# Performance work log

Measured on AMD Instinct MI355X. Metric: run time of the kernel, lower is better.

The kernel has to match this reference:

```python
import jax, jax.numpy as jnp
import numpy as np

TEMPERATURE = 0.07


def setup_inputs() -> dict:
    key = jax.random.key(0)
    k1, k2 = jax.random.split(key)
    features = jax.random.normal(k1, (8192, 512), dtype=jnp.float32)
    targets = jax.random.randint(k2, (8192,), 0, 100, dtype=jnp.int64)
    return {"features": features, "targets": targets}


def reference(features, targets):
    n = features.shape[0]
    # L2 normalize along feature dim (F.normalize, dim=1)
    feats = features / jnp.linalg.norm(features, axis=1, keepdims=True)
    # [N, N] similarity matrix
    sim = jnp.matmul(feats, feats.T) / TEMPERATURE
    # positive-pair mask (same label, excluding self)
    mask = (targets[:, None] == targets[None, :]).astype(sim.dtype)
    mask = mask - jnp.eye(n, dtype=sim.dtype)
    # log_prob = sim - log(sum_j exp(sim_ij)) ; denominator includes the diagonal,
    # exactly as in the torch code. logsumexp is the stable single-pass form.
    log_prob = sim - jax.nn.logsumexp(sim, axis=1, keepdims=True)
    mean_log_prob_pos = jnp.sum(mask * log_prob, axis=1) / jnp.sum(mask, axis=1)
    loss = -jnp.mean(mean_log_prob_pos)
    return loss
```

## Files before the change

kernel.cpp:

```cpp
#include <hip/hip_runtime.h>

#define BM 128
#define BN 128
#define HBN 64
#define NSPLIT 8
#define TEMP 0.07f

typedef __attribute__((ext_vector_type(4))) float f32x4;
typedef __attribute__((ext_vector_type(4))) int   i32x4;
typedef __attribute__((ext_vector_type(8))) int   i32x8;

__global__ __launch_bounds__(256) void knorm(const float* __restrict__ X,
                                             unsigned char* __restrict__ Fq, int D) {
  int row = blockIdx.x * 4 + (threadIdx.x >> 6);
  int lane = threadIdx.x & 63;
  const float4* xr = (const float4*)(X + (size_t)row * D);
  float4 a = xr[lane * 2];
  float4 b = xr[lane * 2 + 1];
  float ss = a.x*a.x + a.y*a.y + a.z*a.z + a.w*a.w
           + b.x*b.x + b.y*b.y + b.z*b.z + b.w*b.w;
  #pragma unroll
  for (int off = 1; off < 64; off <<= 1) ss += __shfl_xor(ss, off, 64);
  float r = rsqrtf(ss);
  int lo = 0, hi = 0;
  lo = __builtin_amdgcn_cvt_pk_fp8_f32(a.x*r, a.y*r, lo, false);
  lo = __builtin_amdgcn_cvt_pk_fp8_f32(a.z*r, a.w*r, lo, true);
  hi = __builtin_amdgcn_cvt_pk_fp8_f32(b.x*r, b.y*r, hi, false);
  hi = __builtin_amdgcn_cvt_pk_fp8_f32(b.z*r, b.w*r, hi, true);
  int2 o = make_int2(lo, hi);
  *(int2*)(Fq + (size_t)row * D + lane * 8) = o;
}

__global__ __launch_bounds__(256, 1)
void kmain(const unsigned char* __restrict__ F, const int* __restrict__ tgt,
           float* __restrict__ psum, float* __restrict__ pmask, int N, int D) {
  __shared__ __align__(16) unsigned char Bs[2][HBN * 512];
  __shared__ int tgts[1024];

  const int tid  = threadIdx.x;
  const int lane = tid & 63;
  const int wave = tid >> 6;
  const int quad = lane >> 4;
  const int l15  = lane & 15;

  const int rowblk   = blockIdx.x / NSPLIT;
  const int split    = blockIdx.x % NSPLIT;
  const int rowbase  = rowblk * BM;
  const int colbase0 = split * (N / NSPLIT);
  const int NS       = N / NSPLIT;
  const int GT       = NS / HBN;

  i32x8 af[2][4];
  #pragma unroll
  for (int mi = 0; mi < 2; ++mi) {
    const unsigned char* rp = F + (size_t)(rowbase + wave*32 + mi*16 + l15) * 512 + quad*32;
    #pragma unroll
    for (int ks = 0; ks < 4; ++ks) {
      i32x4 lo = *(const i32x4*)(rp + ks*128);
      i32x4 hi = *(const i32x4*)(rp + ks*128 + 16);
      af[mi][ks] = __builtin_shufflevector(lo, hi, 0,1,2,3,4,5,6,7);
    }
  }

  int trow[2][4];
  #pragma unroll
  for (int mi = 0; mi < 2; ++mi)
    #pragma unroll
    for (int r = 0; r < 4; ++r)
      trow[mi][r] = tgt[rowbase + wave*32 + mi*16 + quad*4 + r];

  for (int i = tid; i < NS; i += 256) tgts[i] = tgt[colbase0 + i];

  float se[2][4], ms[2][4];
  #pragma unroll
  for (int mi = 0; mi < 2; ++mi)
    #pragma unroll
    for (int r = 0; r < 4; ++r) { se[mi][r] = 0.f; ms[mi][r] = 0.f; }

  const float C1 = (1.0f / TEMP) * 1.4426950408889634f;
  const float C0 = -C1;

  auto STAGE = [&](int g, int buf) {
    const int cb = colbase0 + g * HBN;
    #pragma unroll
    for (int it = 0; it < 8; ++it) {
      const int L   = it * 256 + tid;
      const int row = L >> 5;
      const int ks  = (L & 31) ^ (row & 7);
      const unsigned char* gp = F + (size_t)(cb + row) * 512 + ks * 16;
      __builtin_amdgcn_global_load_lds(
          (const __attribute__((address_space(1))) void*)gp,
          (__attribute__((address_space(3))) void*)(&Bs[buf][0] + L * 16), 16, 0, 0);
    }
  };

  const int sw0 = (quad * 2) ^ (l15 & 7);

  __syncthreads();

  STAGE(0, 0);

  for (int g = 0; g < GT; ++g) {
    if (g + 1 < GT) {
      STAGE(g + 1, (g + 1) & 1);
      asm volatile("s_waitcnt vmcnt(8)" ::: "memory");
    } else {
      asm volatile("s_waitcnt vmcnt(0)" ::: "memory");
    }
    __builtin_amdgcn_s_barrier();

    f32x4 acc[2][4];
    #pragma unroll
    for (int mi = 0; mi < 2; ++mi)
      #pragma unroll
      for (int ni = 0; ni < 4; ++ni)
        acc[mi][ni] = (f32x4){0.f, 0.f, 0.f, 0.f};

    const unsigned char* bb  = &Bs[0][0] + (g & 1) * (HBN * 512) + l15 * 512;
    const unsigned char* bp0 = bb + sw0 * 16;
    const unsigned char* bp1 = bb + (sw0 ^ 1) * 16;

    #pragma unroll
    for (int ks = 0; ks < 4; ++ks) {
      #pragma unroll
      for (int ni = 0; ni < 4; ++ni) {
        i32x4 b0 = *(const i32x4*)(bp0 + ni*8192 + ks*128);
        i32x4 b1 = *(const i32x4*)(bp1 + ni*8192 + ks*128);
        i32x8 b = __builtin_shufflevector(b0, b1, 0,1,2,3,4,5,6,7);
        acc[0][ni] = __builtin_amdgcn_mfma_scale_f32_16x16x128_f8f6f4(
            af[0][ks], b, acc[0][ni], 0, 0, 0, 0x7F7F7F7F, 0, 0x7F7F7F7F);
        acc[1][ni] = __builtin_amdgcn_mfma_scale_f32_16x16x128_f8f6f4(
            af[1][ks], b, acc[1][ni], 0, 0, 0, 0x7F7F7F7F, 0, 0x7F7F7F7F);
      }
    }
    __builtin_amdgcn_s_barrier();

    int tc[4];
    #pragma unroll
    for (int ni = 0; ni < 4; ++ni) tc[ni] = tgts[g*HBN + ni*16 + l15];
    #pragma unroll
    for (int mi = 0; mi < 2; ++mi)
      #pragma unroll
      for (int ni = 0; ni < 4; ++ni)
        #pragma unroll
        for (int r = 0; r < 4; ++r) {
          float v = acc[mi][ni][r];
          se[mi][r] += __builtin_amdgcn_exp2f(fmaf(v, C1, C0));
          if (tc[ni] == trow[mi][r]) ms[mi][r] += v;
        }
  }

  #pragma unroll
  for (int mi = 0; mi < 2; ++mi)
    #pragma unroll
    for (int r = 0; r < 4; ++r) {
      float s = se[mi][r], m = ms[mi][r];
      #pragma unroll
      for (int off = 1; off < 16; off <<= 1) {
        s += __shfl_xor(s, off, 64);
        m += __shfl_xor(m, off, 64);
      }
      if (l15 == 0) {
        int row = rowbase + wave*32 + mi*16 + quad*4 + r;
        psum[(size_t)split * N + row]  = s;
        pmask[(size_t)split * N + row] = m;
      }
    }
}

__global__ __launch_bounds__(256) void kfinal(
    const float* __restrict__ psum, const float* __restrict__ pmask,
    const int* __restrict__ tgt, float* __restrict__ out, int N) {
  __shared__ int h[128];
  __shared__ float wsum[4];
  const int tid = threadIdx.x;
  if (tid < 128) h[tid] = 0;
  __syncthreads();
  for (int i = tid; i < N; i += 256) atomicAdd(&h[tgt[i] & 127], 1);
  __syncthreads();

  const int i = blockIdx.x * 256 + tid;
  float s = 0.f, m = 0.f;
  #pragma unroll
  for (int sp = 0; sp < NSPLIT; ++sp) {
    s += psum[(size_t)sp * N + i];
    m += pmask[(size_t)sp * N + i];
  }
  const float invT = 1.0f / TEMP;
  float cnt = (float)(h[tgt[i] & 127] - 1);
  float term = (m - 1.0f) * invT / cnt - (logf(s) + invT);
  #pragma unroll
  for (int off = 1; off < 64; off <<= 1) term += __shfl_xor(term, off, 64);
  if ((tid & 63) == 0) wsum[tid >> 6] = term;
  __syncthreads();
  if (tid == 0)
    atomicAdd(out, -(wsum[0] + wsum[1] + wsum[2] + wsum[3]) / (float)N);
}

extern "C" void kernel_launch(void* const* d_in, const int* in_sizes, int n_in,
                              void* d_out, int out_size, void* d_ws, size_t ws_size,
                              hipStream_t stream) {
  const float* X  = (const float*)d_in[0];
  const int* tgt  = (const int*)d_in[1];
  float* out      = (float*)d_out;
  const int N = in_sizes[1];
  const int D = in_sizes[0] / N;

  char* w = (char*)d_ws;
  unsigned char* Fq = (unsigned char*)w;
  size_t off = (size_t)N * D;
  float* psum  = (float*)(w + off); off += (size_t)NSPLIT * N * sizeof(float);
  float* pmask = (float*)(w + off);

  hipMemsetAsync(d_out, 0, sizeof(float), stream);
  knorm<<<N / 4, 256, 0, stream>>>(X, Fq, D);
  kmain<<<(N / BM) * NSPLIT, 256, 0, stream>>>(Fq, tgt, psum, pmask, N, D);
  kfinal<<<N / 256, 256, 0, stream>>>(psum, pmask, tgt, out, N);
}
```

Baseline: 114.9 us.

## Exploit similarity symmetry: compute only upper-triangular tiles with column-side reductions

The main kernel now computes only the upper-triangular 128x128 tile pairs of the symmetric similarity matrix. Each tile produces row sums for block I and, when off-diagonal, column sums for block J, written into per-block partial slots, which roughly halves the MFMA and exp work. In exchange there are more, smaller blocks, each loading a 128-column tile up front without a pipelined loop, plus extra column reductions through LDS. The final kernel now sums over 64 partial slots instead of 8, and the normalization kernel uses a coalesced row layout.

After: 151.4 us. 1.32x slower.

```diff
diff --git a/kernel.cpp b/kernel.cpp
--- a/kernel.cpp
+++ b/kernel.cpp
@@ -1,9 +1,7 @@
 #include <hip/hip_runtime.h>
 
 #define BM 128
-#define BN 128
 #define HBN 64
-#define NSPLIT 8
 #define TEMP 0.07f
 
 typedef __attribute__((ext_vector_type(4))) float f32x4;
@@ -15,8 +13,8 @@
   int row = blockIdx.x * 4 + (threadIdx.x >> 6);
   int lane = threadIdx.x & 63;
   const float4* xr = (const float4*)(X + (size_t)row * D);
-  float4 a = xr[lane * 2];
-  float4 b = xr[lane * 2 + 1];
+  float4 a = xr[lane];
+  float4 b = xr[lane + 64];
   float ss = a.x*a.x + a.y*a.y + a.z*a.z + a.w*a.w
            + b.x*b.x + b.y*b.y + b.z*b.z + b.w*b.w;
   #pragma unroll
@@ -27,15 +25,16 @@
   lo = __builtin_amdgcn_cvt_pk_fp8_f32(a.z*r, a.w*r, lo, true);
   hi = __builtin_amdgcn_cvt_pk_fp8_f32(b.x*r, b.y*r, hi, false);
   hi = __builtin_amdgcn_cvt_pk_fp8_f32(b.z*r, b.w*r, hi, true);
-  int2 o = make_int2(lo, hi);
-  *(int2*)(Fq + (size_t)row * D + lane * 8) = o;
+  unsigned char* op = Fq + (size_t)row * D;
+  *(int*)(op + lane * 4)       = lo;
+  *(int*)(op + 256 + lane * 4) = hi;
 }
 
 __global__ __launch_bounds__(256, 1)
 void kmain(const unsigned char* __restrict__ F, const int* __restrict__ tgt,
            float* __restrict__ psum, float* __restrict__ pmask, int N, int D) {
   __shared__ __align__(16) unsigned char Bs[2][HBN * 512];
-  __shared__ int tgts[1024];
+  __shared__ float cred[2][4][128];
 
   const int tid  = threadIdx.x;
   const int lane = tid & 63;
@@ -43,12 +42,21 @@
   const int quad = lane >> 4;
   const int l15  = lane & 15;
 
-  const int rowblk   = blockIdx.x / NSPLIT;
-  const int split    = blockIdx.x % NSPLIT;
-  const int rowbase  = rowblk * BM;
-  const int colbase0 = split * (N / NSPLIT);
-  const int NS       = N / NSPLIT;
-  const int GT       = NS / HBN;
+  const int NBLK = N / BM;
+  const int half = NBLK >> 1;
+  const int base = NBLK * half;
+  int I, J;
+  if ((int)blockIdx.x < base) {
+    int t = blockIdx.x / NBLK;
+    I = blockIdx.x - t * NBLK;
+    J = I + t; if (J >= NBLK) J -= NBLK;
+  } else {
+    I = blockIdx.x - base;
+    J = I + half;
+  }
+  const bool diag = (I == J);
+  const int rowbase = I * BM;
+  const int colbase = J * BM;
 
   i32x8 af[2][4];
   #pragma unroll
@@ -69,46 +77,37 @@
     for (int r = 0; r < 4; ++r)
       trow[mi][r] = tgt[rowbase + wave*32 + mi*16 + quad*4 + r];
 
-  for (int i = tid; i < NS; i += 256) tgts[i] = tgt[colbase0 + i];
+  int tc0[4], tc1[4];
+  #pragma unroll
+  for (int ni = 0; ni < 4; ++ni) {
+    tc0[ni] = tgt[colbase + ni*16 + l15];
+    tc1[ni] = tgt[colbase + 64 + ni*16 + l15];
+  }
+
+  #pragma unroll
+  for (int it = 0; it < 16; ++it) {
+    const int L   = it * 256 + tid;
+    const int row = L >> 5;
+    const int ks  = (L & 31) ^ (row & 7);
+    const unsigned char* gp = F + (size_t)(colbase + row) * 512 + ks * 16;
+    __builtin_amdgcn_global_load_lds(
+        (const __attribute__((address_space(1))) void*)gp,
+        (__attribute__((address_space(3))) void*)(&Bs[0][0] + L * 16), 16, 0, 0);
+  }
 
   float se[2][4], ms[2][4];
   #pragma unroll
   for (int mi = 0; mi < 2; ++mi)
     #pragma unroll
     for (int r = 0; r < 4; ++r) { se[mi][r] = 0.f; ms[mi][r] = 0.f; }
+  f32x4 ce0 = (f32x4){0,0,0,0}, ce1 = (f32x4){0,0,0,0};
+  f32x4 cm0 = (f32x4){0,0,0,0}, cm1 = (f32x4){0,0,0,0};
 
   const float C1 = (1.0f / TEMP) * 1.4426950408889634f;
   const float C0 = -C1;
-
-  auto STAGE = [&](int g, int buf) {
-    const int cb = colbase0 + g * HBN;
-    #pragma unroll
-    for (int it = 0; it < 8; ++it) {
-      const int L   = it * 256 + tid;
-      const int row = L >> 5;
-      const int ks  = (L & 31) ^ (row & 7);
-      const unsigned char* gp = F + (size_t)(cb + row) * 512 + ks * 16;
-      __builtin_amdgcn_global_load_lds(
-          (const __attribute__((address_space(1))) void*)gp,
-          (__attribute__((address_space(3))) void*)(&Bs[buf][0] + L * 16), 16, 0, 0);
-    }
-  };
-
   const int sw0 = (quad * 2) ^ (l15 & 7);
 
-  __syncthreads();
-
-  STAGE(0, 0);
-
-  for (int g = 0; g < GT; ++g) {
-    if (g + 1 < GT) {
-      STAGE(g + 1, (g + 1) & 1);
-      asm volatile("s_waitcnt vmcnt(8)" ::: "memory");
-    } else {
-      asm volatile("s_waitcnt vmcnt(0)" ::: "memory");
-    }
-    __builtin_amdgcn_s_barrier();
-
+  auto PHASE = [&](const int g, f32x4& ceg, f32x4& cmg, const int (&tcg)[4]) {
     f32x4 acc[2][4];
     #pragma unroll
     for (int mi = 0; mi < 2; ++mi)
@@ -116,7 +115,7 @@
       for (int ni = 0; ni < 4; ++ni)
         acc[mi][ni] = (f32x4){0.f, 0.f, 0.f, 0.f};
 
-    const unsigned char* bb  = &Bs[0][0] + (g & 1) * (HBN * 512) + l15 * 512;
+    const unsigned char* bb  = &Bs[0][0] + g * (HBN * 512) + l15 * 512;
     const unsigned char* bp0 = bb + sw0 * 16;
     const unsigned char* bp1 = bb + (sw0 ^ 1) * 16;
 
@@ -133,11 +132,7 @@
             af[1][ks], b, acc[1][ni], 0, 0, 0, 0x7F7F7F7F, 0, 0x7F7F7F7F);
       }
     }
-    __builtin_amdgcn_s_barrier();
-
-    int tc[4];
-    #pragma unroll
-    for (int ni = 0; ni < 4; ++ni) tc[ni] = tgts[g*HBN + ni*16 + l15];
+
     #pragma unroll
     for (int mi = 0; mi < 2; ++mi)
       #pragma unroll
@@ -145,10 +140,19 @@
         #pragma unroll
         for (int r = 0; r < 4; ++r) {
           float v = acc[mi][ni][r];
-          se[mi][r] += __builtin_amdgcn_exp2f(fmaf(v, C1, C0));
-          if (tc[ni] == trow[mi][r]) ms[mi][r] += v;
+          float e = __builtin_amdgcn_exp2f(fmaf(v, C1, C0));
+          se[mi][r] += e;
+          ceg[ni]   += e;
+          if (tcg[ni] == trow[mi][r]) { ms[mi][r] += v; cmg[ni] += v; }
         }
-  }
+  };
+
+  asm volatile("s_waitcnt vmcnt(8)" ::: "memory");
+  __builtin_amdgcn_s_barrier();
+  PHASE(0, ce0, cm0, tc0);
+  asm volatile("s_waitcnt vmcnt(0)" ::: "memory");
+  __builtin_amdgcn_s_barrier();
+  PHASE(1, ce1, cm1, tc1);
 
   #pragma unroll
   for (int mi = 0; mi < 2; ++mi)
@@ -162,15 +166,38 @@
       }
       if (l15 == 0) {
         int row = rowbase + wave*32 + mi*16 + quad*4 + r;
-        psum[(size_t)split * N + row]  = s;
-        pmask[(size_t)split * N + row] = m;
+        psum [(size_t)J * N + row] = s;
+        pmask[(size_t)J * N + row] = m;
       }
     }
+
+  if (!diag) {
+    #pragma unroll
+    for (int g = 0; g < 2; ++g)
+      #pragma unroll
+      for (int ni = 0; ni < 4; ++ni) {
+        float e = g ? ce1[ni] : ce0[ni];
+        float m = g ? cm1[ni] : cm0[ni];
+        e += __shfl_xor(e, 16, 64); e += __shfl_xor(e, 32, 64);
+        m += __shfl_xor(m, 16, 64); m += __shfl_xor(m, 32, 64);
+        if (quad == 0) {
+          cred[0][wave][g*64 + ni*16 + l15] = e;
+          cred[1][wave][g*64 + ni*16 + l15] = m;
+        }
+      }
+  }
+  __syncthreads();
+  if (!diag && tid < 128) {
+    float s = cred[0][0][tid] + cred[0][1][tid] + cred[0][2][tid] + cred[0][3][tid];
+    float m = cred[1][0][tid] + cred[1][1][tid] + cred[1][2][tid] + cred[1][3][tid];
+    psum [(size_t)I * N + colbase + tid] = s;
+    pmask[(size_t)I * N + colbase + tid] = m;
+  }
 }
 
 __global__ __launch_bounds__(256) void kfinal(
     const float* __restrict__ psum, const float* __restrict__ pmask,
-    const int* __restrict__ tgt, float* __restrict__ out, int N) {
+    const int* __restrict__ tgt, float* __restrict__ out, int N, int nslot) {
   __shared__ int h[128];
   __shared__ float wsum[4];
   const int tid = threadIdx.x;
@@ -181,8 +208,8 @@
 
   const int i = blockIdx.x * 256 + tid;
   float s = 0.f, m = 0.f;
-  #pragma unroll
-  for (int sp = 0; sp < NSPLIT; ++sp) {
+  #pragma unroll 8
+  for (int sp = 0; sp < nslot; ++sp) {
     s += psum[(size_t)sp * N + i];
     m += pmask[(size_t)sp * N + i];
   }
@@ -205,15 +232,17 @@
   float* out      = (float*)d_out;
   const int N = in_sizes[1];
   const int D = in_sizes[0] / N;
+  const int NBLK = N / BM;
+  const int grid2 = NBLK * (NBLK + 1) / 2;
 
   char* w = (char*)d_ws;
   unsigned char* Fq = (unsigned char*)w;
   size_t off = (size_t)N * D;
-  float* psum  = (float*)(w + off); off += (size_t)NSPLIT * N * sizeof(float);
+  float* psum  = (float*)(w + off); off += (size_t)NBLK * N * sizeof(float);
   float* pmask = (float*)(w + off);
 
   hipMemsetAsync(d_out, 0, sizeof(float), stream);
   knorm<<<N / 4, 256, 0, stream>>>(X, Fq, D);
-  kmain<<<(N / BM) * NSPLIT, 256, 0, stream>>>(Fq, tgt, psum, pmask, N, D);
-  kfinal<<<N / 256, 256, 0, stream>>>(psum, pmask, tgt, out, N);
-}
+  kmain<<<grid2, 256, 0, stream>>>(Fq, tgt, psum, pmask, N, D);
+  kfinal<<<N / 256, 256, 0, stream>>>(psum, pmask, tgt, out, N, NBLK);
+}
```

## Software-pipeline exp epilogue behind next tile's MFMAs, fold memset into norm kernel

Applied to the files above, without the earlier changes.

The main loop now processes the previous tile's accumulators (exp2 and the positive-mask sum) at the top of the next iteration, so the transcendental work can overlap with the MFMA issue of the current tile. The MFMA block is raised to high wave priority with s_setprio. A dummy zero tile in the first iteration is cancelled by subtracting its exp contribution at the end. The norm kernel also zeroes the output, which removes the separate memset launch, and it uses coalesced float4 loads with a permuted fp8 column order. That permutation is the same for every row, so the dot products are unchanged. The cost is more live registers for the carried accumulators, and the dummy-subtraction trick adds a small floating-point error.

Result: no change. 116.1 us (+1.0%).

```diff
diff --git a/kernel.cpp b/kernel.cpp
--- a/kernel.cpp
+++ b/kernel.cpp
@@ -1,7 +1,6 @@
 #include <hip/hip_runtime.h>
 
 #define BM 128
-#define BN 128
 #define HBN 64
 #define NSPLIT 8
 #define TEMP 0.07f
@@ -11,12 +10,14 @@
 typedef __attribute__((ext_vector_type(8))) int   i32x8;
 
 __global__ __launch_bounds__(256) void knorm(const float* __restrict__ X,
-                                             unsigned char* __restrict__ Fq, int D) {
+                                             unsigned char* __restrict__ Fq,
+                                             float* __restrict__ out, int D) {
+  if (blockIdx.x == 0 && threadIdx.x == 0) *out = 0.f;
   int row = blockIdx.x * 4 + (threadIdx.x >> 6);
   int lane = threadIdx.x & 63;
   const float4* xr = (const float4*)(X + (size_t)row * D);
-  float4 a = xr[lane * 2];
-  float4 b = xr[lane * 2 + 1];
+  float4 a = xr[lane];
+  float4 b = xr[lane + 64];
   float ss = a.x*a.x + a.y*a.y + a.z*a.z + a.w*a.w
            + b.x*b.x + b.y*b.y + b.z*b.z + b.w*b.w;
   #pragma unroll
@@ -27,8 +28,9 @@
   lo = __builtin_amdgcn_cvt_pk_fp8_f32(a.z*r, a.w*r, lo, true);
   hi = __builtin_amdgcn_cvt_pk_fp8_f32(b.x*r, b.y*r, hi, false);
   hi = __builtin_amdgcn_cvt_pk_fp8_f32(b.z*r, b.w*r, hi, true);
-  int2 o = make_int2(lo, hi);
-  *(int2*)(Fq + (size_t)row * D + lane * 8) = o;
+  unsigned char* op = Fq + (size_t)row * D;
+  *(int*)(op + lane * 4)       = lo;
+  *(int*)(op + 256 + lane * 4) = hi;
 }
 
 __global__ __launch_bounds__(256, 1)
@@ -96,6 +98,16 @@
 
   const int sw0 = (quad * 2) ^ (l15 & 7);
 
+  f32x4 accP[2][4];
+  int   tcP[4];
+  #pragma unroll
+  for (int mi = 0; mi < 2; ++mi)
+    #pragma unroll
+    for (int ni = 0; ni < 4; ++ni)
+      accP[mi][ni] = (f32x4){0.f, 0.f, 0.f, 0.f};
+  #pragma unroll
+  for (int ni = 0; ni < 4; ++ni) tcP[ni] = trow[0][0];
+
   __syncthreads();
 
   STAGE(0, 0);
@@ -109,6 +121,17 @@
     }
     __builtin_amdgcn_s_barrier();
 
+    #pragma unroll
+    for (int mi = 0; mi < 2; ++mi)
+      #pragma unroll
+      for (int ni = 0; ni < 4; ++ni)
+        #pragma unroll
+        for (int r = 0; r < 4; ++r) {
+          float v = accP[mi][ni][r];
+          se[mi][r] += __builtin_amdgcn_exp2f(fmaf(v, C1, C0));
+          if (tcP[ni] == trow[mi][r]) ms[mi][r] += v;
+        }
+
     f32x4 acc[2][4];
     #pragma unroll
     for (int mi = 0; mi < 2; ++mi)
@@ -120,6 +143,7 @@
     const unsigned char* bp0 = bb + sw0 * 16;
     const unsigned char* bp1 = bb + (sw0 ^ 1) * 16;
 
+    __builtin_amdgcn_s_setprio(1);
     #pragma unroll
     for (int ks = 0; ks < 4; ++ks) {
       #pragma unroll
@@ -133,21 +157,35 @@
             af[1][ks], b, acc[1][ni], 0, 0, 0, 0x7F7F7F7F, 0, 0x7F7F7F7F);
       }
     }
+    __builtin_amdgcn_s_setprio(0);
+
+    #pragma unroll
+    for (int mi = 0; mi < 2; ++mi)
+      #pragma unroll
+      for (int ni = 0; ni < 4; ++ni)
+        accP[mi][ni] = acc[mi][ni];
+    #pragma unroll
+    for (int ni = 0; ni < 4; ++ni) tcP[ni] = tgts[g*HBN + ni*16 + l15];
+
     __builtin_amdgcn_s_barrier();
-
-    int tc[4];
-    #pragma unroll
-    for (int ni = 0; ni < 4; ++ni) tc[ni] = tgts[g*HBN + ni*16 + l15];
-    #pragma unroll
-    for (int mi = 0; mi < 2; ++mi)
-      #pragma unroll
-      for (int ni = 0; ni < 4; ++ni)
-        #pragma unroll
-        for (int r = 0; r < 4; ++r) {
-          float v = acc[mi][ni][r];
-          se[mi][r] += __builtin_amdgcn_exp2f(fmaf(v, C1, C0));
-          if (tc[ni] == trow[mi][r]) ms[mi][r] += v;
-        }
+  }
+
+  #pragma unroll
+  for (int mi = 0; mi < 2; ++mi)
+    #pragma unroll
+    for (int ni = 0; ni < 4; ++ni)
+      #pragma unroll
+      for (int r = 0; r < 4; ++r) {
+        float v = accP[mi][ni][r];
+        se[mi][r] += __builtin_amdgcn_exp2f(fmaf(v, C1, C0));
+        if (tcP[ni] == trow[mi][r]) ms[mi][r] += v;
+      }
+  {
+    float dummy = 16.0f * __builtin_amdgcn_exp2f(C0);
+    #pragma unroll
+    for (int mi = 0; mi < 2; ++mi)
+      #pragma unroll
+      for (int r = 0; r < 4; ++r) se[mi][r] -= dummy;
   }
 
   #pragma unroll
@@ -212,8 +250,7 @@
   float* psum  = (float*)(w + off); off += (size_t)NSPLIT * N * sizeof(float);
   float* pmask = (float*)(w + off);
 
-  hipMemsetAsync(d_out, 0, sizeof(float), stream);
-  knorm<<<N / 4, 256, 0, stream>>>(X, Fq, D);
+  knorm<<<N / 4, 256, 0, stream>>>(X, Fq, out, D);
   kmain<<<(N / BM) * NSPLIT, 256, 0, stream>>>(Fq, tgt, psum, pmask, N, D);
   kfinal<<<N / 256, 256, 0, stream>>>(psum, pmask, tgt, out, N);
 }
```
